# Kernel optimization log

Hardware: AMD Instinct MI355X
Metric: run time of the kernel (lower is better)

## Reference

```python
import jax, jax.numpy as jnp
import numpy as np

N = 4096
Q0, Q1 = 1000, 500  # number of groups per random-effect factor
LOG_2PI = float(np.log(2.0 * np.pi))


def setup_inputs() -> dict:
    key = jax.random.key(0)
    k1, k2, k3, k4 = jax.random.split(key, 4)
    y_true = jax.random.normal(k1, (N, 1), dtype=jnp.float32)
    y_pred = jax.random.normal(k2, (N, 1), dtype=jnp.float32)
    Z_idx0 = jax.random.randint(k3, (N,), 0, Q0, dtype=jnp.int64)
    Z_idx1 = jax.random.randint(k4, (N,), 0, Q1, dtype=jnp.int64)
    sig2e = jnp.ones((1,), dtype=jnp.float32)
    sig2bs = jnp.ones((2,), dtype=jnp.float32)
    return {"y_true": y_true, "y_pred": y_pred, "Z_idx0": Z_idx0,
            "Z_idx1": Z_idx1, "sig2e": sig2e, "sig2bs": sig2bs}


def reference(y_true, y_pred, Z_idx0, Z_idx1, sig2e, sig2bs):
    n = y_true.shape[0]
    dtype = y_true.dtype
    # V = sig2e * I + sum_k sig2bs[k] * Z_k Z_k^T.
    # For one-hot Z built from group indices, (Z Z^T)[i,j] = 1[idx_i == idx_j],
    # so we form it directly without materializing the [N, q] one-hot.
    V = sig2e[0] * jnp.eye(n, dtype=dtype)
    for k, idx in enumerate((Z_idx0, Z_idx1)):
        same_group = (idx[:, None] == idx[None, :]).astype(dtype)  # [N, N]
        V = V + sig2bs[k] * same_group
    V_inv = jnp.linalg.inv(V)
    r = y_true - y_pred                         # [N, 1]
    loss2 = r.T @ (V_inv @ r)                   # [1, 1] quadratic form
    _, logdet = jnp.linalg.slogdet(V)           # log(det(V)); V is SPD
    total_loss = 0.5 * n * LOG_2PI + 0.5 * logdet + 0.5 * loss2
    return total_loss  # [1, 1]
```

## Files before the change

kernel.cpp:

```cpp
#include <hip/hip_runtime.h>
#include <math.h>


constexpr int N_PTS = 4096;
constexpr int Q0 = 1000;
constexpr int Q1 = 500;
constexpr int QP = 512;
constexpr float LOG_2PI = 1.8378770664093453f;
constexpr float KAPPA = 16384.f;

constexpr int OFF_C0   = 0;
constexpr int OFF_C1   = 1024;
constexpr int OFF_U0   = 2048;
constexpr int OFF_U1   = 3072;
constexpr int OFF_SC   = 3584;
constexpr int OFF_BAR  = 3596;
constexpr int ZERO_FLOATS = 3600;
constexpr int OFF_OFFS = 3600;
constexpr int OFF_CURS = 4624;
constexpr int OFF_SRT  = 5648;
constexpr int OFF_S    = 10240;
constexpr int NB_CHOL  = 28;

__device__ __forceinline__ float readlane_f(float v, int l) {
    return __int_as_float(__builtin_amdgcn_readlane(__float_as_int(v), l));
}

__global__ __launch_bounds__(256) void k_scatter(const float* __restrict__ yt,
                                                 const float* __restrict__ yp,
                                                 const int* __restrict__ z0,
                                                 const int* __restrict__ z1,
                                                 float* __restrict__ ws) {
    int i = blockIdx.x * blockDim.x + threadIdx.x;
    float r = 0.f;
    if (i < N_PTS) {
        r = yt[i] - yp[i];
        int i0 = z0[i];
        int i1 = z1[i];
        atomicAdd(&ws[OFF_C0 + i0], 1.0f);
        atomicAdd(&ws[OFF_C1 + i1], 1.0f);
        atomicAdd(&ws[OFF_U0 + i0], r);
        atomicAdd(&ws[OFF_U1 + i1], r);
    }
    float r2 = r * r;
    #pragma unroll
    for (int off = 32; off; off >>= 1) r2 += __shfl_down(r2, off, 64);
    if ((threadIdx.x & 63) == 0) atomicAdd(&ws[OFF_SC + 0], r2);
}

__global__ __launch_bounds__(1024) void k_prefix(float* __restrict__ ws) {
    __shared__ int lds[1024];
    int tid = threadIdx.x;
    int v = (tid < Q0) ? (int)ws[OFF_C0 + tid] : 0;
    lds[tid] = v;
    __syncthreads();
    for (int off = 1; off < 1024; off <<= 1) {
        int add = (tid >= off) ? lds[tid - off] : 0;
        __syncthreads();
        lds[tid] += add;
        __syncthreads();
    }
    int excl = lds[tid] - v;
    ((int*)(ws + OFF_OFFS))[tid] = excl;
    ((int*)(ws + OFF_CURS))[tid] = excl;
}

__global__ __launch_bounds__(256) void k_sortscatter(const int* __restrict__ z0,
                                                     const int* __restrict__ z1,
                                                     float* __restrict__ ws) {
    int i = blockIdx.x * blockDim.x + threadIdx.x;
    if (i < N_PTS) {
        int g = z0[i];
        int slot = atomicAdd(&((int*)(ws + OFF_CURS))[g], 1);
        ((int*)(ws + OFF_SRT))[slot] = z1[i];
    }
}

__global__ __launch_bounds__(256) void k_init_s(const float* __restrict__ sig2e,
                                                const float* __restrict__ sig2bs,
                                                float* __restrict__ ws) {
    const float inv_se = 1.f / sig2e[0], inv_sb1 = 1.f / sig2bs[1];
    const float* C1w = ws + OFF_C1;
    const float* U1w = ws + OFF_U1;
    int idx = blockIdx.x * 256 + threadIdx.x;
    int i = idx >> 7;
    int j0 = (idx & 127) << 2;
    float4 v;
    float* e = &v.x;
    #pragma unroll
    for (int t = 0; t < 4; ++t) {
        int j = j0 + t;
        float x = 0.f;
        if (i == 500)      x = (j < Q1) ? U1w[j] : ((j == 500) ? KAPPA : 0.f);
        else if (i == j)   x = (i < Q1) ? (inv_sb1 + C1w[i] * inv_se) : 1.f;
        e[t] = x;
    }
    *reinterpret_cast<float4*>(ws + OFF_S + (size_t)i * QP + j0) = v;
}

__global__ __launch_bounds__(256) void k_pairs(const float* __restrict__ sig2e,
                                               const float* __restrict__ sig2bs,
                                               float* __restrict__ ws) {
    const float inv_se = 1.f / sig2e[0], inv_sb0 = 1.f / sig2bs[0];
    int g = blockIdx.x * 256 + threadIdx.x;
    if (g >= Q0) return;
    const int* offs = (const int*)(ws + OFF_OFFS);
    const int* srt  = (const int*)(ws + OFF_SRT);
    float* S = ws + OFF_S;

    float cg = ws[OFF_C0 + g];
    float a  = inv_sb0 + cg * inv_se;
    float u0 = ws[OFF_U0 + g];
    float wu = u0 / a;
    atomicAdd(&ws[OFF_SC + 1], logf(a));
    atomicAdd(&ws[OFF_SC + 2], u0 * wu);

    int beg = offs[g];
    int cnt = (int)cg;
    float coef = -inv_se * inv_se / a;
    float rhsv = -inv_se * wu;
    for (int ia = beg; ia < beg + cnt; ++ia) {
        int ca = srt[ia];
        atomicAdd(&S[(size_t)500 * QP + ca], rhsv);
        for (int ib = beg; ib < beg + cnt; ++ib) {
            int cb = srt[ib];
            if (ca >= cb) atomicAdd(&S[(size_t)ca * QP + cb], coef);
        }
    }
}

__device__ __forceinline__ void gbar(unsigned* cnt, int* it) {
    __syncthreads();
    if (threadIdx.x == 0) {
        __threadfence();
        atomicAdd(cnt, 1u);
        unsigned target = (unsigned)NB_CHOL * (unsigned)(++(*it));
        while (atomicAdd(cnt, 0u) < target) __builtin_amdgcn_s_sleep(2);
        __threadfence();
    }
    __syncthreads();
}

__device__ __forceinline__ void chol64_store(float (&d)[64], float* S, int base, int lane) {
    #pragma unroll
    for (int j = 0; j < 64; ++j) {
        float diag = readlane_f(d[j], j);
        float rs = rsqrtf(diag);
        d[j] *= rs;
        float lj = d[j];
        #pragma unroll
        for (int k = j + 1; k < 64; ++k)
            d[k] = fmaf(-lj, readlane_f(lj, k), d[k]);
    }
    float* wr = S + (size_t)(base + lane) * QP + base;
    #pragma unroll
    for (int c = 0; c < 16; ++c) {
        float4 v;
        v.x = (4 * c + 0 <= lane) ? d[4 * c + 0] : 0.f;
        v.y = (4 * c + 1 <= lane) ? d[4 * c + 1] : 0.f;
        v.z = (4 * c + 2 <= lane) ? d[4 * c + 2] : 0.f;
        v.w = (4 * c + 3 <= lane) ? d[4 * c + 3] : 0.f;
        *reinterpret_cast<float4*>(wr + 4 * c) = v;
    }
}

__device__ __forceinline__ void solve_tile(const float* S, int x, int g0,
                                           float (*out)[65], int lane) {
    float dreg[64], p[64];
    const float* dr = S + (size_t)(x + lane) * QP + x;
    const float* pr = S + (size_t)(g0 + lane) * QP + x;
    #pragma unroll
    for (int c = 0; c < 16; ++c) {
        float4 v = *reinterpret_cast<const float4*>(dr + 4 * c);
        dreg[4 * c] = v.x; dreg[4 * c + 1] = v.y; dreg[4 * c + 2] = v.z; dreg[4 * c + 3] = v.w;
        float4 q = *reinterpret_cast<const float4*>(pr + 4 * c);
        p[4 * c] = q.x; p[4 * c + 1] = q.y; p[4 * c + 2] = q.z; p[4 * c + 3] = q.w;
    }
    #pragma unroll
    for (int j = 0; j < 64; ++j) {
        float diag = readlane_f(dreg[j], j);
        float pj = p[j] / diag;
        p[j] = pj;
        #pragma unroll
        for (int k = j + 1; k < 64; ++k)
            p[k] = fmaf(-pj, readlane_f(dreg[j], k), p[k]);
    }
    #pragma unroll
    for (int k = 0; k < 64; ++k) out[lane][k] = p[k];
}

__global__ __launch_bounds__(256) void k_chol(const float* __restrict__ sig2e,
                                              const float* __restrict__ sig2bs,
                                              float* __restrict__ ws,
                                              float* __restrict__ out) {
    float* S = ws + OFF_S;
    unsigned* bar = (unsigned*)(ws + OFF_BAR);
    const int tid = threadIdx.x;
    const int lane = tid & 63;
    const int w = tid >> 6;
    const int blk = blockIdx.x;
    __shared__ float Pi[64][65];
    __shared__ float Pj[64][65];
    int bit = 0;

    if (blk == 0 && w == 0) {
        float d[64];
        const float* row = S + (size_t)lane * QP;
        #pragma unroll
        for (int c = 0; c < 16; ++c) {
            float4 v = *reinterpret_cast<const float4*>(row + 4 * c);
            d[4 * c] = v.x; d[4 * c + 1] = v.y; d[4 * c + 2] = v.z; d[4 * c + 3] = v.w;
        }
        chol64_store(d, S, 0, lane);
    }
    gbar(bar, &bit);

    for (int s = 0; s < 7; ++s) {
        const int x = 64 * s;
        const int T = 7 - s;
        const int nt = T * (T + 1) / 2;
        if (blk < nt) {
            int ti = 0;
            while ((ti + 1) * (ti + 2) / 2 <= blk) ++ti;
            int tj = blk - ti * (ti + 1) / 2;
            const int gi0 = x + 64 + 64 * ti;
            const int gj0 = x + 64 + 64 * tj;

            if (w == 0)                     solve_tile(S, x, gi0, Pi, lane);
            else if (w == 1 && ti != tj)    solve_tile(S, x, gj0, Pj, lane);
            __syncthreads();

            float (*PJ)[65] = (ti == tj) ? Pi : Pj;
            const int ta = tid >> 4, tb = tid & 15;
            float acc[4][4] = {{0.f}};
            #pragma unroll
            for (int j = 0; j < 64; ++j) {
                float pa[4], pb[4];
                #pragma unroll
                for (int u = 0; u < 4; ++u) { pa[u] = Pi[ta * 4 + u][j]; pb[u] = PJ[tb * 4 + u][j]; }
                #pragma unroll
                for (int u = 0; u < 4; ++u)
                    #pragma unroll
                    for (int v = 0; v < 4; ++v) acc[u][v] += pa[u] * pb[v];
            }

            if (ti > tj) {
                #pragma unroll
                for (int u = 0; u < 4; ++u) {
                    float4* ptr = (float4*)&S[(size_t)(gi0 + ta * 4 + u) * QP + gj0 + tb * 4];
                    float4 cv = *ptr;
                    cv.x -= acc[u][0]; cv.y -= acc[u][1]; cv.z -= acc[u][2]; cv.w -= acc[u][3];
                    *ptr = cv;
                }
            } else {
                float nv[4][4];
                #pragma unroll
                for (int u = 0; u < 4; ++u) {
                    float4 cv = *(const float4*)&S[(size_t)(gi0 + ta * 4 + u) * QP + gj0 + tb * 4];
                    nv[u][0] = cv.x - acc[u][0]; nv[u][1] = cv.y - acc[u][1];
                    nv[u][2] = cv.z - acc[u][2]; nv[u][3] = cv.w - acc[u][3];
                }
                #pragma unroll
                for (int u = 0; u < 4; ++u)
                    #pragma unroll
                    for (int v = 0; v < 4; ++v) {
                        int gi = gi0 + ta * 4 + u, gj = gj0 + tb * 4 + v;
                        if (gi >= gj) S[(size_t)gi * QP + gj] = nv[u][v];
                    }
                if (ti == 0) {
                    #pragma unroll
                    for (int u = 0; u < 4; ++u)
                        #pragma unroll
                        for (int v = 0; v < 4; ++v)
                            Pj[ta * 4 + u][tb * 4 + v] = nv[u][v];
                }
            }

            if (blk == 0) {
                __syncthreads();
                if (w == 0) {
                    float d[64];
                    #pragma unroll
                    for (int k = 0; k < 64; ++k) d[k] = Pj[lane][k];
                    chol64_store(d, S, x + 64, lane);
                }
            }
        }
        gbar(bar, &bit);
    }

    if (blk == 0) {
        const float se = sig2e[0], sb0 = sig2bs[0], sb1 = sig2bs[1];
        const float inv_se = 1.f / se;
        float ld = 0.f;
        for (int i = tid; i < Q1; i += 256) ld += logf(S[(size_t)i * QP + i]);
        float* red = &Pi[0][0];
        __syncthreads();
        red[tid] = ld;
        __syncthreads();
        if (tid < 128) red[tid] += red[tid + 128];
        __syncthreads();
        if (tid < 64) red[tid] += red[tid + 64];
        __syncthreads();
        if (tid < 64) {
            float v = red[tid];
            #pragma unroll
            for (int o = 32; o; o >>= 1) v += __shfl_down(v, o, 64);
            if (tid == 0) {
                float L55 = S[(size_t)500 * QP + 500];
                float zz = KAPPA - L55 * L55;
                float rtr = ws[OFF_SC + 0];
                float la  = ws[OFF_SC + 1];
                float q0p = ws[OFF_SC + 2];
                float umu = q0p + zz;
                float loss2 = inv_se * rtr - inv_se * inv_se * umu;
                float logdetV = (float)N_PTS * logf(se)
                              + (float)Q0 * logf(sb0)
                              + (float)Q1 * logf(sb1)
                              + la + 2.f * v;
                out[0] = 0.5f * ((float)N_PTS * LOG_2PI + logdetV + loss2);
            }
        }
    }
}

extern "C" void kernel_launch(void* const* d_in, const int* in_sizes, int n_in,
                              void* d_out, int out_size, void* d_ws, size_t ws_size,
                              hipStream_t stream) {
    const float* yt = (const float*)d_in[0];
    const float* yp = (const float*)d_in[1];
    const int*   z0 = (const int*)d_in[2];
    const int*   z1 = (const int*)d_in[3];
    const float* se = (const float*)d_in[4];
    const float* sb = (const float*)d_in[5];
    float* ws  = (float*)d_ws;
    float* out = (float*)d_out;

    hipMemsetAsync(d_ws, 0, (size_t)ZERO_FLOATS * sizeof(float), stream);
    hipLaunchKernelGGL(k_scatter, dim3(N_PTS / 256), dim3(256), 0, stream, yt, yp, z0, z1, ws);
    hipLaunchKernelGGL(k_prefix, dim3(1), dim3(1024), 0, stream, ws);
    hipLaunchKernelGGL(k_sortscatter, dim3(N_PTS / 256), dim3(256), 0, stream, z0, z1, ws);
    hipLaunchKernelGGL(k_init_s, dim3(QP * QP / 4 / 256), dim3(256), 0, stream, se, sb, ws);
    hipLaunchKernelGGL(k_pairs, dim3(4), dim3(256), 0, stream, se, sb, ws);
    hipLaunchKernelGGL(k_chol, dim3(NB_CHOL), dim3(256), 0, stream, se, sb, ws, out);
}
```

Measured before the change: 396.3 us.

## Fuse preprocessing kernels into two grid-barrier kernels and use precomputed inverse diagonals

Merges the scatter, prefix-sum and sort-scatter stages into one persistent kernel separated by grid barriers. The S initialization and pair-accumulation steps move into the Cholesky kernel, so six launches become two. The triangular solve now multiplies by stored reciprocal square roots of the diagonal instead of dividing. This removes launch gaps at the cost of extra grid barriers, and it assumes all blocks are co-resident.

```diff
diff --git a/kernel.cpp b/kernel.cpp
--- a/kernel.cpp
+++ b/kernel.cpp
@@ -14,144 +14,107 @@
 constexpr int OFF_U0   = 2048;
 constexpr int OFF_U1   = 3072;
 constexpr int OFF_SC   = 3584;
-constexpr int OFF_BAR  = 3596;
-constexpr int ZERO_FLOATS = 3600;
-constexpr int OFF_OFFS = 3600;
-constexpr int OFF_CURS = 4624;
-constexpr int OFF_SRT  = 5648;
-constexpr int OFF_S    = 10240;
+constexpr int OFF_BARP = 3616;
+constexpr int OFF_BARC = 3648;
+constexpr int ZERO_FLOATS = 3680;
+constexpr int OFF_INVD = 3712;
+constexpr int OFF_OFFS = 4608;
+constexpr int OFF_CURS = 5632;
+constexpr int OFF_SRT  = 6656;
+constexpr int OFF_S    = 12288;
+constexpr int NB_PRE   = 16;
 constexpr int NB_CHOL  = 28;
 
 __device__ __forceinline__ float readlane_f(float v, int l) {
     return __int_as_float(__builtin_amdgcn_readlane(__float_as_int(v), l));
 }
 
-__global__ __launch_bounds__(256) void k_scatter(const float* __restrict__ yt,
-                                                 const float* __restrict__ yp,
-                                                 const int* __restrict__ z0,
-                                                 const int* __restrict__ z1,
-                                                 float* __restrict__ ws) {
-    int i = blockIdx.x * blockDim.x + threadIdx.x;
-    float r = 0.f;
-    if (i < N_PTS) {
-        r = yt[i] - yp[i];
-        int i0 = z0[i];
-        int i1 = z1[i];
-        atomicAdd(&ws[OFF_C0 + i0], 1.0f);
-        atomicAdd(&ws[OFF_C1 + i1], 1.0f);
-        atomicAdd(&ws[OFF_U0 + i0], r);
-        atomicAdd(&ws[OFF_U1 + i1], r);
-    }
-    float r2 = r * r;
-    #pragma unroll
-    for (int off = 32; off; off >>= 1) r2 += __shfl_down(r2, off, 64);
-    if ((threadIdx.x & 63) == 0) atomicAdd(&ws[OFF_SC + 0], r2);
-}
-
-__global__ __launch_bounds__(1024) void k_prefix(float* __restrict__ ws) {
-    __shared__ int lds[1024];
-    int tid = threadIdx.x;
-    int v = (tid < Q0) ? (int)ws[OFF_C0 + tid] : 0;
-    lds[tid] = v;
-    __syncthreads();
-    for (int off = 1; off < 1024; off <<= 1) {
-        int add = (tid >= off) ? lds[tid - off] : 0;
-        __syncthreads();
-        lds[tid] += add;
-        __syncthreads();
-    }
-    int excl = lds[tid] - v;
-    ((int*)(ws + OFF_OFFS))[tid] = excl;
-    ((int*)(ws + OFF_CURS))[tid] = excl;
-}
-
-__global__ __launch_bounds__(256) void k_sortscatter(const int* __restrict__ z0,
-                                                     const int* __restrict__ z1,
-                                                     float* __restrict__ ws) {
-    int i = blockIdx.x * blockDim.x + threadIdx.x;
-    if (i < N_PTS) {
-        int g = z0[i];
-        int slot = atomicAdd(&((int*)(ws + OFF_CURS))[g], 1);
-        ((int*)(ws + OFF_SRT))[slot] = z1[i];
-    }
-}
-
-__global__ __launch_bounds__(256) void k_init_s(const float* __restrict__ sig2e,
-                                                const float* __restrict__ sig2bs,
-                                                float* __restrict__ ws) {
-    const float inv_se = 1.f / sig2e[0], inv_sb1 = 1.f / sig2bs[1];
-    const float* C1w = ws + OFF_C1;
-    const float* U1w = ws + OFF_U1;
-    int idx = blockIdx.x * 256 + threadIdx.x;
-    int i = idx >> 7;
-    int j0 = (idx & 127) << 2;
-    float4 v;
-    float* e = &v.x;
-    #pragma unroll
-    for (int t = 0; t < 4; ++t) {
-        int j = j0 + t;
-        float x = 0.f;
-        if (i == 500)      x = (j < Q1) ? U1w[j] : ((j == 500) ? KAPPA : 0.f);
-        else if (i == j)   x = (i < Q1) ? (inv_sb1 + C1w[i] * inv_se) : 1.f;
-        e[t] = x;
-    }
-    *reinterpret_cast<float4*>(ws + OFF_S + (size_t)i * QP + j0) = v;
-}
-
-__global__ __launch_bounds__(256) void k_pairs(const float* __restrict__ sig2e,
-                                               const float* __restrict__ sig2bs,
-                                               float* __restrict__ ws) {
-    const float inv_se = 1.f / sig2e[0], inv_sb0 = 1.f / sig2bs[0];
-    int g = blockIdx.x * 256 + threadIdx.x;
-    if (g >= Q0) return;
-    const int* offs = (const int*)(ws + OFF_OFFS);
-    const int* srt  = (const int*)(ws + OFF_SRT);
-    float* S = ws + OFF_S;
-
-    float cg = ws[OFF_C0 + g];
-    float a  = inv_sb0 + cg * inv_se;
-    float u0 = ws[OFF_U0 + g];
-    float wu = u0 / a;
-    atomicAdd(&ws[OFF_SC + 1], logf(a));
-    atomicAdd(&ws[OFF_SC + 2], u0 * wu);
-
-    int beg = offs[g];
-    int cnt = (int)cg;
-    float coef = -inv_se * inv_se / a;
-    float rhsv = -inv_se * wu;
-    for (int ia = beg; ia < beg + cnt; ++ia) {
-        int ca = srt[ia];
-        atomicAdd(&S[(size_t)500 * QP + ca], rhsv);
-        for (int ib = beg; ib < beg + cnt; ++ib) {
-            int cb = srt[ib];
-            if (ca >= cb) atomicAdd(&S[(size_t)ca * QP + cb], coef);
-        }
-    }
-}
-
-__device__ __forceinline__ void gbar(unsigned* cnt, int* it) {
+__device__ __forceinline__ void gbar(unsigned* cnt, int* it, int nb) {
     __syncthreads();
     if (threadIdx.x == 0) {
         __threadfence();
-        atomicAdd(cnt, 1u);
-        unsigned target = (unsigned)NB_CHOL * (unsigned)(++(*it));
-        while (atomicAdd(cnt, 0u) < target) __builtin_amdgcn_s_sleep(2);
+        __hip_atomic_fetch_add(cnt, 1u, __ATOMIC_RELAXED, __HIP_MEMORY_SCOPE_AGENT);
+        unsigned target = (unsigned)nb * (unsigned)(++(*it));
+        while (__hip_atomic_load(cnt, __ATOMIC_RELAXED, __HIP_MEMORY_SCOPE_AGENT) < target)
+            __builtin_amdgcn_s_sleep(8);
         __threadfence();
     }
     __syncthreads();
 }
 
-__device__ __forceinline__ void chol64_store(float (&d)[64], float* S, int base, int lane) {
+__global__ __launch_bounds__(256) void k_pre(const float* __restrict__ yt,
+                                             const float* __restrict__ yp,
+                                             const int* __restrict__ z0,
+                                             const int* __restrict__ z1,
+                                             float* __restrict__ ws) {
+    unsigned* bar = (unsigned*)(ws + OFF_BARP);
+    int it = 0;
+    const int tid = threadIdx.x;
+    const int i = blockIdx.x * 256 + tid;
+
+    float r = yt[i] - yp[i];
+    int i0 = z0[i];
+    int i1 = z1[i];
+    atomicAdd(&ws[OFF_C0 + i0], 1.0f);
+    atomicAdd(&ws[OFF_C1 + i1], 1.0f);
+    atomicAdd(&ws[OFF_U0 + i0], r);
+    atomicAdd(&ws[OFF_U1 + i1], r);
+    float r2 = r * r;
+    #pragma unroll
+    for (int off = 32; off; off >>= 1) r2 += __shfl_down(r2, off, 64);
+    if ((tid & 63) == 0) atomicAdd(&ws[OFF_SC + 0], r2);
+
+    gbar(bar, &it, NB_PRE);
+
+    if (blockIdx.x == 0) {
+        __shared__ int sums[256];
+        int b4 = tid * 4;
+        int v[4], tot = 0;
+        #pragma unroll
+        for (int k = 0; k < 4; ++k) {
+            v[k] = (b4 + k < Q0) ? (int)ws[OFF_C0 + b4 + k] : 0;
+            tot += v[k];
+        }
+        sums[tid] = tot;
+        __syncthreads();
+        for (int off = 1; off < 256; off <<= 1) {
+            int a = (tid >= off) ? sums[tid - off] : 0;
+            __syncthreads();
+            sums[tid] += a;
+            __syncthreads();
+        }
+        int run = sums[tid] - tot;
+        int* offs = (int*)(ws + OFF_OFFS);
+        int* curs = (int*)(ws + OFF_CURS);
+        #pragma unroll
+        for (int k = 0; k < 4; ++k) {
+            offs[b4 + k] = run;
+            curs[b4 + k] = run;
+            run += v[k];
+        }
+    }
+
+    gbar(bar, &it, NB_PRE);
+
+    int slot = atomicAdd(&((int*)(ws + OFF_CURS))[i0], 1);
+    ((int*)(ws + OFF_SRT))[slot] = i1;
+}
+
+__device__ __forceinline__ void chol64_store(float (&d)[64], float* S, float* invd,
+                                             int base, int lane) {
+    float myinv = 0.f;
     #pragma unroll
     for (int j = 0; j < 64; ++j) {
         float diag = readlane_f(d[j], j);
         float rs = rsqrtf(diag);
+        if (lane == j) myinv = rs;
         d[j] *= rs;
         float lj = d[j];
         #pragma unroll
         for (int k = j + 1; k < 64; ++k)
             d[k] = fmaf(-lj, readlane_f(lj, k), d[k]);
     }
+    invd[base + lane] = myinv;
     float* wr = S + (size_t)(base + lane) * QP + base;
     #pragma unroll
     for (int c = 0; c < 16; ++c) {
@@ -164,8 +127,9 @@
     }
 }
 
-__device__ __forceinline__ void solve_tile(const float* S, int x, int g0,
-                                           float (*out)[65], int lane) {
+__device__ __forceinline__ void solve_tile(const float* S, const float* invd,
+                                           int x, int g0, float (*out)[65], int lane) {
+    float invv = invd[x + lane];
     float dreg[64], p[64];
     const float* dr = S + (size_t)(x + lane) * QP + x;
     const float* pr = S + (size_t)(g0 + lane) * QP + x;
@@ -178,8 +142,7 @@
     }
     #pragma unroll
     for (int j = 0; j < 64; ++j) {
-        float diag = readlane_f(dreg[j], j);
-        float pj = p[j] / diag;
+        float pj = p[j] * readlane_f(invv, j);
         p[j] = pj;
         #pragma unroll
         for (int k = j + 1; k < 64; ++k)
@@ -194,7 +157,8 @@
                                               float* __restrict__ ws,
                                               float* __restrict__ out) {
     float* S = ws + OFF_S;
-    unsigned* bar = (unsigned*)(ws + OFF_BAR);
+    float* invd = ws + OFF_INVD;
+    unsigned* bar = (unsigned*)(ws + OFF_BARC);
     const int tid = threadIdx.x;
     const int lane = tid & 63;
     const int w = tid >> 6;
@@ -203,6 +167,57 @@
     __shared__ float Pj[64][65];
     int bit = 0;
 
+    const float se = sig2e[0], sb0 = sig2bs[0], sb1 = sig2bs[1];
+    const float inv_se = 1.f / se, inv_sb0 = 1.f / sb0, inv_sb1 = 1.f / sb1;
+
+    {
+        const float* C1w = ws + OFF_C1;
+        const float* U1w = ws + OFF_U1;
+        for (int e = blk * 256 + tid; e < QP * QP / 4; e += NB_CHOL * 256) {
+            int i = e >> 7;
+            int j0 = (e & 127) << 2;
+            float4 v;
+            float* el = &v.x;
+            #pragma unroll
+            for (int t = 0; t < 4; ++t) {
+                int j = j0 + t;
+                float x = 0.f;
+                if (i == 500)      x = (j < Q1) ? U1w[j] : ((j == 500) ? KAPPA : 0.f);
+                else if (i == j)   x = (i < Q1) ? (inv_sb1 + C1w[i] * inv_se) : 1.f;
+                el[t] = x;
+            }
+            *reinterpret_cast<float4*>(S + (size_t)i * QP + j0) = v;
+        }
+    }
+    gbar(bar, &bit, NB_CHOL);
+
+    {
+        int g = blk * 256 + tid;
+        if (g < Q0) {
+            const int* offs = (const int*)(ws + OFF_OFFS);
+            const int* srt  = (const int*)(ws + OFF_SRT);
+            float cg = ws[OFF_C0 + g];
+            float a  = inv_sb0 + cg * inv_se;
+            float u0 = ws[OFF_U0 + g];
+            float wu = u0 / a;
+            atomicAdd(&ws[OFF_SC + 1], logf(a));
+            atomicAdd(&ws[OFF_SC + 2], u0 * wu);
+            int beg = offs[g];
+            int cnt = (int)cg;
+            float coef = -inv_se * inv_se / a;
+            float rhsv = -inv_se * wu;
+            for (int ia = beg; ia < beg + cnt; ++ia) {
+                int ca = srt[ia];
+                atomicAdd(&S[(size_t)500 * QP + ca], rhsv);
+                for (int ib = beg; ib < beg + cnt; ++ib) {
+                    int cb = srt[ib];
+                    if (ca >= cb) atomicAdd(&S[(size_t)ca * QP + cb], coef);
+                }
+            }
+        }
+    }
+    gbar(bar, &bit, NB_CHOL);
+
     if (blk == 0 && w == 0) {
         float d[64];
         const float* row = S + (size_t)lane * QP;
@@ -211,9 +226,9 @@
             float4 v = *reinterpret_cast<const float4*>(row + 4 * c);
             d[4 * c] = v.x; d[4 * c + 1] = v.y; d[4 * c + 2] = v.z; d[4 * c + 3] = v.w;
         }
-        chol64_store(d, S, 0, lane);
-    }
-    gbar(bar, &bit);
+        chol64_store(d, S, invd, 0, lane);
+    }
+    gbar(bar, &bit, NB_CHOL);
 
     for (int s = 0; s < 7; ++s) {
         const int x = 64 * s;
@@ -226,8 +241,8 @@
             const int gi0 = x + 64 + 64 * ti;
             const int gj0 = x + 64 + 64 * tj;
 
-            if (w == 0)                     solve_tile(S, x, gi0, Pi, lane);
-            else if (w == 1 && ti != tj)    solve_tile(S, x, gj0, Pj, lane);
+            if (w == 0)                     solve_tile(S, invd, x, gi0, Pi, lane);
+            else if (w == 1 && ti != tj)    solve_tile(S, invd, x, gj0, Pj, lane);
             __syncthreads();
 
             float (*PJ)[65] = (ti == tj) ? Pi : Pj;
@@ -282,16 +297,14 @@
                     float d[64];
                     #pragma unroll
                     for (int k = 0; k < 64; ++k) d[k] = Pj[lane][k];
-                    chol64_store(d, S, x + 64, lane);
-                }
-            }
-        }
-        gbar(bar, &bit);
+                    chol64_store(d, S, invd, x + 64, lane);
+                }
+            }
+        }
+        gbar(bar, &bit, NB_CHOL);
     }
 
     if (blk == 0) {
-        const float se = sig2e[0], sb0 = sig2bs[0], sb1 = sig2bs[1];
-        const float inv_se = 1.f / se;
         float ld = 0.f;
         for (int i = tid; i < Q1; i += 256) ld += logf(S[(size_t)i * QP + i]);
         float* red = &Pi[0][0];
@@ -337,10 +350,6 @@
     float* out = (float*)d_out;
 
     hipMemsetAsync(d_ws, 0, (size_t)ZERO_FLOATS * sizeof(float), stream);
-    hipLaunchKernelGGL(k_scatter, dim3(N_PTS / 256), dim3(256), 0, stream, yt, yp, z0, z1, ws);
-    hipLaunchKernelGGL(k_prefix, dim3(1), dim3(1024), 0, stream, ws);
-    hipLaunchKernelGGL(k_sortscatter, dim3(N_PTS / 256), dim3(256), 0, stream, z0, z1, ws);
-    hipLaunchKernelGGL(k_init_s, dim3(QP * QP / 4 / 256), dim3(256), 0, stream, se, sb, ws);
-    hipLaunchKernelGGL(k_pairs, dim3(4), dim3(256), 0, stream, se, sb, ws);
+    hipLaunchKernelGGL(k_pre, dim3(NB_PRE), dim3(256), 0, stream, yt, yp, z0, z1, ws);
     hipLaunchKernelGGL(k_chol, dim3(NB_CHOL), dim3(256), 0, stream, se, sb, ws, out);
 }
```

Result: slower. 420.6 us (+6.1%).
